# Kernel optimization log

Measured on AMD Instinct MI355X. Metric: run time of the kernel, lower is better.

## Reference

```python
import jax, jax.numpy as jnp
import numpy as np

NUM_GROUPS = 8   # also the per-group channel count (C = NUM_GROUPS**2)
NUM_LEVELS = 4
RADIUS = 4


def setup_inputs() -> dict:
    key = jax.random.key(0)
    k1, k2, k3 = jax.random.split(key, 3)
    B, C, H, W = 2, 64, 80, 160
    fmap1 = jax.random.normal(k1, (B, C, H, W), dtype=jnp.float32)
    fmap2 = jax.random.normal(k2, (B, C, H, W), dtype=jnp.float32)
    coords = jax.random.uniform(k3, (B, 1, H, W), dtype=jnp.float32) * (W - 1)
    return {"fmap1": fmap1, "fmap2": fmap2, "coords": coords}


def _build_cost_volume(fmap1, fmap2):
    # group-wise correlation: torch.split(fmap, G, dim=1) -> chunks of G channels
    B, C, H, W = fmap1.shape
    G = NUM_GROUPS
    gc = NUM_GROUPS  # chunk size; C == G * gc
    f1 = fmap1.reshape(B, G, gc, H, W)
    f2 = fmap2.reshape(B, G, gc, H, W)
    # cv[b,g,h,w,v] = sum_c f1[b,g,c,h,w] * f2[b,g,c,h,v] / sqrt(gc)
    cv = jnp.einsum('bgchw,bgchv->bghwv', f1, f2) / jnp.sqrt(jnp.float32(gc))
    return cv  # (B, G, H, W, W2)


def _pyramid(cv, n_levels):
    pyr = [cv]
    for _ in range(n_levels):
        B, G, H, W, Wl = cv.shape
        cv = cv.reshape(B, G, H, W, Wl // 2, 2).mean(-1)  # avg_pool1d(k=2,s=2)
        pyr.append(cv)
    return pyr


def _linear_sample(cv, x):
    # cv: (B,G,H,W,Wl) 1D signals; x: (B,G,H,W,K) sample positions
    Wl = cv.shape[-1]
    x0 = jnp.floor(x)
    w1 = x - x0
    i0 = x0.astype(jnp.int32)
    i1 = i0 + 1
    g0 = jnp.take_along_axis(cv, jnp.clip(i0, 0, Wl - 1), axis=-1)
    g1 = jnp.take_along_axis(cv, jnp.clip(i1, 0, Wl - 1), axis=-1)
    v0 = (i0 >= 0) & (i0 < Wl)
    v1 = (i1 >= 0) & (i1 < Wl)
    zero = jnp.zeros((), cv.dtype)
    return jnp.where(v0, g0 * (1.0 - w1), zero) + jnp.where(v1, g1 * w1, zero)


def reference(fmap1, fmap2, coords):
    B, _, H, W = coords.shape
    G, r = NUM_GROUPS, RADIUS
    K = 2 * r + 1
    cv = _build_cost_volume(fmap1, fmap2)
    geo = cv  # regularizer_3d treated as identity (see notes)
    feat_pyr = _pyramid(cv, NUM_LEVELS)
    geo_pyr = _pyramid(geo, NUM_LEVELS)
    dx = jnp.linspace(-r, r, K, dtype=jnp.float32)  # (K,)
    c = coords[:, 0][:, None]  # (B,1,H,W), broadcasts over groups
    outs = []
    for i in range(NUM_LEVELS):
        coords_lvl = c[..., None] / (2.0 ** i) + dx  # (B,1,H,W,K)
        coords_lvl = jnp.broadcast_to(coords_lvl, (B, G, H, W, K))
        for pyr in (feat_pyr, geo_pyr):
            s = _linear_sample(pyr[i], coords_lvl)            # (B,G,H,W,K)
            outs.append(s.transpose(0, 2, 3, 1, 4).reshape(B, H, W, G * K))
    out = jnp.concatenate(outs, axis=-1)  # (B,H,W, 2*L*G*K)
    return out.transpose(0, 3, 1, 2).astype(jnp.float32)
```

## Files before the change

kernel.cpp:

```cpp
#include <hip/hip_runtime.h>


namespace {
constexpr int B_ = 2, C_ = 64, H_ = 80, W_ = 160;
constexpr int G_ = 8, GC_ = 8, L_ = 4, K_ = 9, R_ = 4;
constexpr int HW_ = H_ * W_;
constexpr int NCH_ = 2 * L_ * G_ * K_;
constexpr int TPB = 192;
constexpr float INV_SQRT_GC = 0.35355339059327373f;
}

__device__ __forceinline__ float dot8(const float* p, const float* f) {
  float4 a = *(const float4*)(p);
  float4 b = *(const float4*)(p + 4);
  return f[0] * a.x + f[1] * a.y + f[2] * a.z + f[3] * a.w +
         f[4] * b.x + f[5] * b.y + f[6] * b.z + f[7] * b.w;
}

__global__ __launch_bounds__(TPB) void gacv_kernel(
    const float* __restrict__ fmap1, const float* __restrict__ fmap2,
    const float* __restrict__ coords, float* __restrict__ out) {
  __shared__ __align__(16) float p0[W_ * GC_];
  __shared__ __align__(16) float p1[(W_ / 2) * GC_];
  __shared__ __align__(16) float p2[(W_ / 4) * GC_];
  __shared__ __align__(16) float p3[(W_ / 8) * GC_];

  const int tid = threadIdx.x;
  const int bid = blockIdx.x;
  const int h = bid % H_;
  const int bg = bid / H_;
  const int g = bg % G_;
  const int b = bg / G_;

  const float* f2base = fmap2 + (size_t)(b * C_ + g * GC_) * HW_ + h * W_;
  for (int idx = tid; idx < W_ * GC_; idx += TPB) {
    int v = idx % W_;
    int c = idx / W_;
    p0[v * GC_ + c] = f2base[c * HW_ + v];
  }
  __syncthreads();
  for (int idx = tid; idx < (W_ / 2) * GC_; idx += TPB) {
    int c = idx & (GC_ - 1);
    p1[idx] = 0.5f * (p0[2 * idx - c] + p0[2 * idx - c + GC_]);
  }
  __syncthreads();
  for (int idx = tid; idx < (W_ / 4) * GC_; idx += TPB) {
    int c = idx & (GC_ - 1);
    p2[idx] = 0.5f * (p1[2 * idx - c] + p1[2 * idx - c + GC_]);
  }
  __syncthreads();
  for (int idx = tid; idx < (W_ / 8) * GC_; idx += TPB) {
    int c = idx & (GC_ - 1);
    p3[idx] = 0.5f * (p2[2 * idx - c] + p2[2 * idx - c + GC_]);
  }
  __syncthreads();

  if (tid >= W_) return;
  const int w = tid;

  float f1v[GC_];
  const float* f1base = fmap1 + (size_t)(b * C_ + g * GC_) * HW_ + h * W_ + w;
#pragma unroll
  for (int c = 0; c < GC_; ++c) f1v[c] = f1base[c * HW_] * INV_SQRT_GC;

  const float cx = coords[(b * H_ + h) * W_ + w];
  float* outb = out + (size_t)b * NCH_ * HW_ + h * W_ + w;
  const int gk = g * K_;

  const float* pyrs[4] = {p0, p1, p2, p3};
#pragma unroll
  for (int i = 0; i < L_; ++i) {
    const int Wl = W_ >> i;
    const float xl = cx * (1.0f / (1 << i));
    const float F = floorf(xl);
    const int fi = (int)F;
    const float w1 = xl - F;
    const float w0 = 1.0f - w1;
    const float* pyr = pyrs[i];

    float T[2 * R_ + 2];
#pragma unroll
    for (int j = 0; j < 2 * R_ + 2; ++j) {
      int t = fi - R_ + j;
      int tc = min(max(t, 0), Wl - 1);
      float s = dot8(pyr + tc * GC_, f1v);
      T[j] = (t == tc) ? s : 0.0f;
    }

    const int chBase = (2 * i) * (G_ * K_) + gk;
#pragma unroll
    for (int k = 0; k < K_; ++k) {
      float val = w0 * T[k] + w1 * T[k + 1];
      outb[(size_t)(chBase + k) * HW_] = val;
      outb[(size_t)(chBase + G_ * K_ + k) * HW_] = val;
    }
  }
}

extern "C" void kernel_launch(void* const* d_in, const int* in_sizes, int n_in,
                              void* d_out, int out_size, void* d_ws, size_t ws_size,
                              hipStream_t stream) {
  const float* fmap1 = (const float*)d_in[0];
  const float* fmap2 = (const float*)d_in[1];
  const float* coords = (const float*)d_in[2];
  float* out = (float*)d_out;
  gacv_kernel<<<dim3(B_ * G_ * H_), dim3(TPB), 0, stream>>>(fmap1, fmap2, coords, out);
}
```

Baseline: 85.05 us.

## Split rows into halves and assign one pyramid level per thread

Each block now handles half a row (80 columns) with 320 threads, and each thread computes a single pyramid level instead of looping over all four. The shared pyramid is repacked into two 4-channel planes holding all levels contiguously, and the grid doubles. The aim is more parallelism and fewer idle threads in the compute phase, with shorter per-thread serial work. In exchange, the fmap2 row load and the pyramid build are done twice per row, and fmap1 and coords are read redundantly by each level's thread.

```diff
diff --git a/kernel.cpp b/kernel.cpp
--- a/kernel.cpp
+++ b/kernel.cpp
@@ -6,57 +6,57 @@
 constexpr int G_ = 8, GC_ = 8, L_ = 4, K_ = 9, R_ = 4;
 constexpr int HW_ = H_ * W_;
 constexpr int NCH_ = 2 * L_ * G_ * K_;
-constexpr int TPB = 192;
+constexpr int TPB = 320;
+constexpr int NBINS = 160 + 80 + 40 + 20;
 constexpr float INV_SQRT_GC = 0.35355339059327373f;
 }
 
-__device__ __forceinline__ float dot8(const float* p, const float* f) {
-  float4 a = *(const float4*)(p);
-  float4 b = *(const float4*)(p + 4);
-  return f[0] * a.x + f[1] * a.y + f[2] * a.z + f[3] * a.w +
-         f[4] * b.x + f[5] * b.y + f[6] * b.z + f[7] * b.w;
-}
-
-__global__ __launch_bounds__(TPB) void gacv_kernel(
+__global__ __launch_bounds__(TPB, 5) void gacv_kernel(
     const float* __restrict__ fmap1, const float* __restrict__ fmap2,
     const float* __restrict__ coords, float* __restrict__ out) {
-  __shared__ __align__(16) float p0[W_ * GC_];
-  __shared__ __align__(16) float p1[(W_ / 2) * GC_];
-  __shared__ __align__(16) float p2[(W_ / 4) * GC_];
-  __shared__ __align__(16) float p3[(W_ / 8) * GC_];
+  __shared__ __align__(16) float pA[NBINS * 4];
+  __shared__ __align__(16) float pB[NBINS * 4];
 
   const int tid = threadIdx.x;
   const int bid = blockIdx.x;
-  const int h = bid % H_;
-  const int bg = bid / H_;
+  const int half = bid & 1;
+  const int rid = bid >> 1;
+  const int h = rid % H_;
+  const int bg = rid / H_;
   const int g = bg % G_;
   const int b = bg / G_;
 
   const float* f2base = fmap2 + (size_t)(b * C_ + g * GC_) * HW_ + h * W_;
   for (int idx = tid; idx < W_ * GC_; idx += TPB) {
-    int v = idx % W_;
-    int c = idx / W_;
-    p0[v * GC_ + c] = f2base[c * HW_ + v];
+    int c = idx & 7;
+    int v = idx >> 3;
+    float val = f2base[c * HW_ + v];
+    if (c < 4) pA[v * 4 + c] = val;
+    else       pB[v * 4 + (c - 4)] = val;
   }
   __syncthreads();
-  for (int idx = tid; idx < (W_ / 2) * GC_; idx += TPB) {
-    int c = idx & (GC_ - 1);
-    p1[idx] = 0.5f * (p0[2 * idx - c] + p0[2 * idx - c + GC_]);
+  for (int idx = tid; idx < 80 * 4; idx += TPB) {
+    int t = idx >> 2, c = idx & 3;
+    pA[(160 + t) * 4 + c] = 0.5f * (pA[(2 * t) * 4 + c] + pA[(2 * t + 1) * 4 + c]);
+    pB[(160 + t) * 4 + c] = 0.5f * (pB[(2 * t) * 4 + c] + pB[(2 * t + 1) * 4 + c]);
   }
   __syncthreads();
-  for (int idx = tid; idx < (W_ / 4) * GC_; idx += TPB) {
-    int c = idx & (GC_ - 1);
-    p2[idx] = 0.5f * (p1[2 * idx - c] + p1[2 * idx - c + GC_]);
+  for (int idx = tid; idx < 40 * 4; idx += TPB) {
+    int t = idx >> 2, c = idx & 3;
+    pA[(240 + t) * 4 + c] = 0.5f * (pA[(160 + 2 * t) * 4 + c] + pA[(160 + 2 * t + 1) * 4 + c]);
+    pB[(240 + t) * 4 + c] = 0.5f * (pB[(160 + 2 * t) * 4 + c] + pB[(160 + 2 * t + 1) * 4 + c]);
   }
   __syncthreads();
-  for (int idx = tid; idx < (W_ / 8) * GC_; idx += TPB) {
-    int c = idx & (GC_ - 1);
-    p3[idx] = 0.5f * (p2[2 * idx - c] + p2[2 * idx - c + GC_]);
+  for (int idx = tid; idx < 20 * 4; idx += TPB) {
+    int t = idx >> 2, c = idx & 3;
+    pA[(280 + t) * 4 + c] = 0.5f * (pA[(240 + 2 * t) * 4 + c] + pA[(240 + 2 * t + 1) * 4 + c]);
+    pB[(280 + t) * 4 + c] = 0.5f * (pB[(240 + 2 * t) * 4 + c] + pB[(240 + 2 * t + 1) * 4 + c]);
   }
   __syncthreads();
 
-  if (tid >= W_) return;
-  const int w = tid;
+  const int w_local = tid % 80;
+  const int lvl = tid / 80;
+  const int w = half * 80 + w_local;
 
   float f1v[GC_];
   const float* f1base = fmap1 + (size_t)(b * C_ + g * GC_) * HW_ + h * W_ + w;
@@ -64,36 +64,33 @@
   for (int c = 0; c < GC_; ++c) f1v[c] = f1base[c * HW_] * INV_SQRT_GC;
 
   const float cx = coords[(b * H_ + h) * W_ + w];
+  const float xl = ldexpf(cx, -lvl);
+  const int Wl = W_ >> lvl;
+  const int ofs = (lvl == 0) ? 0 : (lvl == 1) ? 160 : (lvl == 2) ? 240 : 280;
+  const float F = floorf(xl);
+  const int fi = (int)F;
+  const float w1 = xl - F;
+  const float w0 = 1.0f - w1;
+
+  float T[2 * R_ + 2];
+#pragma unroll
+  for (int j = 0; j < 2 * R_ + 2; ++j) {
+    int t = fi - R_ + j;
+    int tc = min(max(t, 0), Wl - 1);
+    const float4 a = *(const float4*)(pA + (ofs + tc) * 4);
+    const float4 q = *(const float4*)(pB + (ofs + tc) * 4);
+    float s = f1v[0] * a.x + f1v[1] * a.y + f1v[2] * a.z + f1v[3] * a.w +
+              f1v[4] * q.x + f1v[5] * q.y + f1v[6] * q.z + f1v[7] * q.w;
+    T[j] = (t == tc) ? s : 0.0f;
+  }
+
   float* outb = out + (size_t)b * NCH_ * HW_ + h * W_ + w;
-  const int gk = g * K_;
-
-  const float* pyrs[4] = {p0, p1, p2, p3};
+  const int chBase = lvl * (2 * G_ * K_) + g * K_;
 #pragma unroll
-  for (int i = 0; i < L_; ++i) {
-    const int Wl = W_ >> i;
-    const float xl = cx * (1.0f / (1 << i));
-    const float F = floorf(xl);
-    const int fi = (int)F;
-    const float w1 = xl - F;
-    const float w0 = 1.0f - w1;
-    const float* pyr = pyrs[i];
-
-    float T[2 * R_ + 2];
-#pragma unroll
-    for (int j = 0; j < 2 * R_ + 2; ++j) {
-      int t = fi - R_ + j;
-      int tc = min(max(t, 0), Wl - 1);
-      float s = dot8(pyr + tc * GC_, f1v);
-      T[j] = (t == tc) ? s : 0.0f;
-    }
-
-    const int chBase = (2 * i) * (G_ * K_) + gk;
-#pragma unroll
-    for (int k = 0; k < K_; ++k) {
-      float val = w0 * T[k] + w1 * T[k + 1];
-      outb[(size_t)(chBase + k) * HW_] = val;
-      outb[(size_t)(chBase + G_ * K_ + k) * HW_] = val;
-    }
+  for (int k = 0; k < K_; ++k) {
+    float val = w0 * T[k] + w1 * T[k + 1];
+    outb[(size_t)(chBase + k) * HW_] = val;
+    outb[(size_t)(chBase + G_ * K_ + k) * HW_] = val;
   }
 }
 
@@ -104,5 +101,5 @@
   const float* fmap2 = (const float*)d_in[1];
   const float* coords = (const float*)d_in[2];
   float* out = (float*)d_out;
-  gacv_kernel<<<dim3(B_ * G_ * H_), dim3(TPB), 0, stream>>>(fmap1, fmap2, coords, out);
+  gacv_kernel<<<dim3(B_ * G_ * H_ * 2), dim3(TPB), 0, stream>>>(fmap1, fmap2, coords, out);
 }
```

New measurement: 86.78 us. +2.0%, slower.
